# Optimization experiments

Measured on AMD Instinct MI355X. Metric: run time of the kernel, lower is better.

The kernel has to match this reference:

```python
import math
import jax, jax.numpy as jnp
import numpy as np

EMBED_DIM = 1024
NUM_HEADS = 16
HEAD_DIM = EMBED_DIM // NUM_HEADS


def _xavier(key, fan_in, fan_out):
    lim = math.sqrt(6.0 / (fan_in + fan_out))
    return jax.random.uniform(key, (fan_out, fan_in), jnp.float32, -lim, lim)


def setup_inputs() -> dict:
    key = jax.random.key(0)
    kx, kq, kk, kv, ko = jax.random.split(key, 5)
    B, L = 4, 2048
    x = jax.random.normal(kx, (B, L, EMBED_DIM), jnp.float32)
    return {
        "x": x,
        "wq": _xavier(kq, EMBED_DIM, EMBED_DIM), "bq": jnp.zeros((EMBED_DIM,), jnp.float32),
        "wk": _xavier(kk, EMBED_DIM, EMBED_DIM), "bk": jnp.zeros((EMBED_DIM,), jnp.float32),
        "wv": _xavier(kv, EMBED_DIM, EMBED_DIM), "bv": jnp.zeros((EMBED_DIM,), jnp.float32),
        "wo": _xavier(ko, EMBED_DIM, EMBED_DIM), "bo": jnp.zeros((EMBED_DIM,), jnp.float32),
    }


def reference(x, wq, bq, wk, bk, wv, bv, wo, bo):
    B, L, D = x.shape
    H, Dh = NUM_HEADS, HEAD_DIM

    def proj(w, b):
        # nn.Linear: x @ w.T + b, then split heads -> (B, H, L, Dh)
        return (jnp.einsum('bld,ed->ble', x, w) + b).reshape(B, L, H, Dh).transpose(0, 2, 1, 3)

    q, k, v = proj(wq, bq), proj(wk, bk), proj(wv, bv)
    # NOTE: original torch code scales by sqrt(key.size(dim=1)) == sqrt(num_heads)
    scale = 1.0 / math.sqrt(H)
    scores = jnp.einsum('bhqd,bhkd->bhqk', q, k) * scale  # (B, H, L, L)
    attn = jax.nn.softmax(scores, axis=-1)
    out = jnp.einsum('bhqk,bhkd->bhqd', attn, v)          # (B, H, L, Dh)
    out = out.transpose(0, 2, 1, 3).reshape(B, L, D)
    return jnp.einsum('bld,ed->ble', out, wo) + bo
```

## Files before the change

kernel.cpp:

```cpp
#include <hip/hip_runtime.h>
#include <hip/hip_bf16.h>

#define DEVI __device__ __forceinline__

using u16 = unsigned short;
typedef __attribute__((ext_vector_type(8))) short bf16x8;
typedef __attribute__((ext_vector_type(4))) short bf16x4;
typedef __attribute__((ext_vector_type(4))) float f32x4;

constexpr int Bb = 4, Ls = 2048, Dd = 1024, Hh = 16, DhC = 64;
constexpr int Mm = Bb * Ls;

DEVI u16 f2bf(float f) {
  union { float f; unsigned u; } x; x.f = f;
  unsigned r = x.u + 0x7FFFu + ((x.u >> 16) & 1u);
  return (u16)(r >> 16);
}
DEVI float bf2f(u16 b) {
  union { unsigned u; float f; } x; x.u = ((unsigned)b) << 16;
  return x.f;
}

DEVI unsigned cvt_pk_bf16(float a, float b) {
  unsigned d;
  asm("v_cvt_pk_bf16_f32 %0, %1, %2" : "=v"(d) : "v"(a), "v"(b));
  return d;
}

DEVI void gload_lds16(const u16* g, u16* l) {
  __builtin_amdgcn_global_load_lds(
      (const __attribute__((address_space(1))) unsigned int*)g,
      (__attribute__((address_space(3))) unsigned int*)l, 16, 0, 0);
}

DEVI bf16x8 ld_frag(const u16* p) { return *reinterpret_cast<const bf16x8*>(p); }

__global__ void cvt_all(const float* __restrict__ x,
                        const float* __restrict__ wq, const float* __restrict__ wk,
                        const float* __restrict__ wv, const float* __restrict__ wo,
                        u16* __restrict__ xb,
                        u16* __restrict__ wqb, u16* __restrict__ wkb,
                        u16* __restrict__ wvb, u16* __restrict__ wob) {
  const int tid = blockIdx.x * blockDim.x + threadIdx.x;
  constexpr int NT = 2048 * 256;
  constexpr int N4X = Mm * Dd / 4;
  constexpr int N4W = Dd * Dd / 4;
  for (int i = tid; i < N4X; i += NT) {
    float4 v = reinterpret_cast<const float4*>(x)[i];
    reinterpret_cast<ushort4*>(xb)[i] =
        make_ushort4(f2bf(v.x), f2bf(v.y), f2bf(v.z), f2bf(v.w));
  }
  for (int i = tid; i < 4 * N4W; i += NT) {
    int which = i / N4W, off = i - which * N4W;
    const float* s = which == 0 ? wq : which == 1 ? wk : which == 2 ? wv : wo;
    u16* d = which == 0 ? wqb : which == 1 ? wkb : which == 2 ? wvb : wob;
    float4 v = reinterpret_cast<const float4*>(s)[off];
    reinterpret_cast<ushort4*>(d)[off] =
        make_ushort4(f2bf(v.x), f2bf(v.y), f2bf(v.z), f2bf(v.w));
  }
}

__global__ __launch_bounds__(256) void gemm_qkv(
    const u16* __restrict__ A, const u16* __restrict__ W,
    const float* __restrict__ bq, const float* __restrict__ bk2,
    const float* __restrict__ bv,
    u16* __restrict__ qm, u16* __restrict__ km, u16* __restrict__ vt)
{
  constexpr int BK = 64, K = 1024;
  __shared__ u16 As[128 * BK];
  __shared__ u16 Bs[128 * BK];
  const int tid = threadIdx.x;
  const int wave = tid >> 6, lane = tid & 63;
  const int wr = wave >> 1, wc = wave & 1;
  const int lrow = lane & 15, lk = (lane >> 4) * 8;
  const int m0 = blockIdx.y * 128;
  const int n0g = blockIdx.x * 128;
  const int srow = lane >> 3, scol = (lane & 7) * 8;

  f32x4 acc[4][4] = {};

  for (int k0 = 0; k0 < K; k0 += BK) {
    __syncthreads();
#pragma unroll
    for (int i = 0; i < 4; ++i) {
      int g = wave * 4 + i;
      int row = g * 8 + srow;
      gload_lds16(A + (size_t)(m0 + row) * K + k0 + scol, As + g * 512);
      gload_lds16(W + (size_t)(n0g + row) * K + k0 + scol, Bs + g * 512);
    }
    __syncthreads();
#pragma unroll
    for (int kk = 0; kk < 2; ++kk) {
      bf16x8 af[4], bfr[4];
#pragma unroll
      for (int m = 0; m < 4; ++m) af[m]  = ld_frag(As + (wr*64 + m*16 + lrow)*BK + kk*32 + lk);
#pragma unroll
      for (int n = 0; n < 4; ++n) bfr[n] = ld_frag(Bs + (wc*64 + n*16 + lrow)*BK + kk*32 + lk);
      __builtin_amdgcn_s_setprio(1);
#pragma unroll
      for (int m = 0; m < 4; ++m)
#pragma unroll
        for (int n = 0; n < 4; ++n)
          acc[m][n] = __builtin_amdgcn_mfma_f32_16x16x32_bf16(af[m], bfr[n], acc[m][n], 0, 0, 0);
      __builtin_amdgcn_s_setprio(0);
    }
  }

  const int region = blockIdx.x >> 3;
  const int nc0 = (blockIdx.x & 7) * 128;
  const float* bias = region == 0 ? bq : region == 1 ? bk2 : bv;
  u16* dstRM = region == 0 ? qm : km;

#pragma unroll
  for (int m = 0; m < 4; ++m) {
#pragma unroll
    for (int n = 0; n < 4; ++n) {
      int row = m0 + wr*64 + m*16 + (lane >> 4) * 4;
      int col = nc0 + wc*64 + n*16 + lrow;
      float bv_ = bias[col];
      if (region == 2) {
        ushort4 o;
        o.x = f2bf(acc[m][n][0] + bv_); o.y = f2bf(acc[m][n][1] + bv_);
        o.z = f2bf(acc[m][n][2] + bv_); o.w = f2bf(acc[m][n][3] + bv_);
        *reinterpret_cast<ushort4*>(&vt[(size_t)col * Mm + row]) = o;
      } else {
#pragma unroll
        for (int j = 0; j < 4; ++j)
          dstRM[(size_t)(row + j) * Dd + col] = f2bf(acc[m][n][j] + bv_);
      }
    }
  }
}

__global__ __launch_bounds__(256) void gemm_out(
    const u16* __restrict__ A, const u16* __restrict__ Bt,
    const float* __restrict__ bias, float* __restrict__ C, int M, int N, int K)
{
  constexpr int BK = 64;
  __shared__ u16 As[128 * BK];
  __shared__ u16 Bs[128 * BK];
  const int tid = threadIdx.x;
  const int wave = tid >> 6, lane = tid & 63;
  const int wr = wave >> 1, wc = wave & 1;
  const int lrow = lane & 15, lk = (lane >> 4) * 8;
  const int m0 = blockIdx.y * 128, n0 = blockIdx.x * 128;
  const int srow = lane >> 3, scol = (lane & 7) * 8;

  f32x4 acc[4][4] = {};

  for (int k0 = 0; k0 < K; k0 += BK) {
    __syncthreads();
#pragma unroll
    for (int i = 0; i < 4; ++i) {
      int g = wave * 4 + i;
      int row = g * 8 + srow;
      gload_lds16(A  + (size_t)(m0 + row) * K + k0 + scol, As + g * 512);
      gload_lds16(Bt + (size_t)(n0 + row) * K + k0 + scol, Bs + g * 512);
    }
    __syncthreads();
#pragma unroll
    for (int kk = 0; kk < 2; ++kk) {
      bf16x8 af[4], bfr[4];
#pragma unroll
      for (int m = 0; m < 4; ++m) af[m]  = ld_frag(As + (wr*64 + m*16 + lrow)*BK + kk*32 + lk);
#pragma unroll
      for (int n = 0; n < 4; ++n) bfr[n] = ld_frag(Bs + (wc*64 + n*16 + lrow)*BK + kk*32 + lk);
      __builtin_amdgcn_s_setprio(1);
#pragma unroll
      for (int m = 0; m < 4; ++m)
#pragma unroll
        for (int n = 0; n < 4; ++n)
          acc[m][n] = __builtin_amdgcn_mfma_f32_16x16x32_bf16(af[m], bfr[n], acc[m][n], 0, 0, 0);
      __builtin_amdgcn_s_setprio(0);
    }
  }

#pragma unroll
  for (int m = 0; m < 4; ++m) {
#pragma unroll
    for (int n = 0; n < 4; ++n) {
      int row = m0 + wr*64 + m*16 + (lane >> 4) * 4;
      int col = n0 + wc*64 + n*16 + lrow;
      float bv = bias[col];
#pragma unroll
      for (int j = 0; j < 4; ++j)
        C[(size_t)(row + j) * N + col] = acc[m][n][j] + bv;
    }
  }
}

__global__ __launch_bounds__(512) void attn_fwd(
    const u16* __restrict__ Qm, const u16* __restrict__ Km,
    const u16* __restrict__ Vt, u16* __restrict__ Om)
{
  __shared__ u16 Ks[2][4096];
  __shared__ u16 Vs[2][4096];

  const int tid = threadIdx.x;
  const int wave = tid >> 6, lane = tid & 63;
  const int lrow = lane & 15, lk = (lane >> 4) * 8;
  const int swz = (lrow & 7) << 3;
  const int b = blockIdx.x >> 4, h = blockIdx.x & 15;
  const int rb = b * Ls;
  const int cb0 = h * DhC;
  const int q0 = blockIdx.y * 128;
  const int srow = lane >> 3;
  const int scol = ((lane & 7) ^ srow) * 8;

  const u16* kg = Km + (size_t)(rb + wave * 8 + srow) * Dd + cb0 + scol;
  const u16* vg = Vt + (size_t)(cb0 + wave * 8 + srow) * Mm + rb + scol;
  u16* ksflat = &Ks[0][0];
  u16* vsflat = &Vs[0][0];
  u16* ksl = ksflat + wave * 512;
  u16* vsl = vsflat + wave * 512;
  constexpr int LBUF = 4096;

#pragma unroll
  for (int g = 0; g < 2; ++g)
    gload_lds16(Qm + (size_t)(rb + q0 + wave * 16 + g * 8 + srow) * Dd + cb0 + scol,
                ksflat + (wave * 2 + g) * 512);
  gload_lds16(vg, vsl);
  __syncthreads();

  constexpr float SCL = 0.25f * 1.44269504088896f;
  bf16x8 aq0 = ld_frag(ksflat + (wave * 16 + lrow) * 64 + (lk ^ swz));
  bf16x8 aq1 = ld_frag(ksflat + (wave * 16 + lrow) * 64 + ((32 + lk) ^ swz));
#pragma unroll
  for (int e = 0; e < 8; e += 2) {
    unsigned d0 = cvt_pk_bf16(SCL * bf2f((u16)aq0[e]), SCL * bf2f((u16)aq0[e + 1]));
    unsigned d1 = cvt_pk_bf16(SCL * bf2f((u16)aq1[e]), SCL * bf2f((u16)aq1[e + 1]));
    aq0[e] = (short)(d0 & 0xffff); aq0[e + 1] = (short)(d0 >> 16);
    aq1[e] = (short)(d1 & 0xffff); aq1[e + 1] = (short)(d1 >> 16);
  }
  __syncthreads();
  gload_lds16(kg, ksl);
  __syncthreads();

  bf16x8 ones;
#pragma unroll
  for (int e = 0; e < 8; ++e) ones[e] = (short)0x3F80;

  f32x4 accO[4] = {};
  f32x4 acc_ps = {};

  int nb = 0;
  for (int kv0 = 0; kv0 < Ls; kv0 += 64) {
    if (kv0 + 64 < Ls) {
      int dst = (nb ^ 1) * LBUF;
      gload_lds16(kg + (size_t)(kv0 + 64) * Dd, ksl + dst);
      gload_lds16(vg + kv0 + 64, vsl + dst);
      asm volatile("s_waitcnt vmcnt(2)" ::: "memory");
    } else {
      asm volatile("s_waitcnt vmcnt(0)" ::: "memory");
    }
    __builtin_amdgcn_s_barrier();
    const u16* ks = ksflat + nb * LBUF;
    const u16* vs = vsflat + nb * LBUF;

    f32x4 s[4];
#pragma unroll
    for (int kb = 0; kb < 4; ++kb) {
      const u16* kr = ks + (kb * 16 + lrow) * 64;
      bf16x8 bk0 = ld_frag(kr + (lk ^ swz));
      bf16x8 bk1 = ld_frag(kr + ((32 + lk) ^ swz));
      f32x4 t = {};
      __builtin_amdgcn_s_setprio(1);
      t = __builtin_amdgcn_mfma_f32_16x16x32_bf16(bk0, aq0, t, 0, 0, 0);
      t = __builtin_amdgcn_mfma_f32_16x16x32_bf16(bk1, aq1, t, 0, 0, 0);
      __builtin_amdgcn_s_setprio(0);
      s[kb] = t;
    }

    unsigned u00 = cvt_pk_bf16(__builtin_amdgcn_exp2f(s[0][0]), __builtin_amdgcn_exp2f(s[0][1]));
    unsigned u01 = cvt_pk_bf16(__builtin_amdgcn_exp2f(s[0][2]), __builtin_amdgcn_exp2f(s[0][3]));
    unsigned u10 = cvt_pk_bf16(__builtin_amdgcn_exp2f(s[1][0]), __builtin_amdgcn_exp2f(s[1][1]));
    unsigned u11 = cvt_pk_bf16(__builtin_amdgcn_exp2f(s[1][2]), __builtin_amdgcn_exp2f(s[1][3]));
    unsigned u20 = cvt_pk_bf16(__builtin_amdgcn_exp2f(s[2][0]), __builtin_amdgcn_exp2f(s[2][1]));
    unsigned u21 = cvt_pk_bf16(__builtin_amdgcn_exp2f(s[2][2]), __builtin_amdgcn_exp2f(s[2][3]));
    unsigned u30 = cvt_pk_bf16(__builtin_amdgcn_exp2f(s[3][0]), __builtin_amdgcn_exp2f(s[3][1]));
    unsigned u31 = cvt_pk_bf16(__builtin_amdgcn_exp2f(s[3][2]), __builtin_amdgcn_exp2f(s[3][3]));

    asm("v_permlane32_swap_b32 %0, %1" : "+v"(u00), "+v"(u10));
    asm("v_permlane16_swap_b32 %0, %1" : "+v"(u00), "+v"(u10));
    asm("v_permlane32_swap_b32 %0, %1" : "+v"(u01), "+v"(u11));
    asm("v_permlane16_swap_b32 %0, %1" : "+v"(u01), "+v"(u11));
    asm("v_permlane32_swap_b32 %0, %1" : "+v"(u20), "+v"(u30));
    asm("v_permlane16_swap_b32 %0, %1" : "+v"(u20), "+v"(u30));
    asm("v_permlane32_swap_b32 %0, %1" : "+v"(u21), "+v"(u31));
    asm("v_permlane16_swap_b32 %0, %1" : "+v"(u21), "+v"(u31));

    union { unsigned u[4]; bf16x8 v; } apc0, apc1;
    apc0.u[0] = u00; apc0.u[1] = u01; apc0.u[2] = u10; apc0.u[3] = u11;
    apc1.u[0] = u20; apc1.u[1] = u21; apc1.u[2] = u30; apc1.u[3] = u31;

#pragma unroll
    for (int kk2 = 0; kk2 < 2; ++kk2) {
      bf16x8 ap = kk2 == 0 ? apc0.v : apc1.v;
      __builtin_amdgcn_s_setprio(1);
#pragma unroll
      for (int cb = 0; cb < 4; ++cb) {
        const u16* vr = vs + (cb * 16 + lrow) * 64;
        bf16x8 bv = ld_frag(vr + ((kk2 * 32 + lk) ^ swz));
        accO[cb] = __builtin_amdgcn_mfma_f32_16x16x32_bf16(bv, ap, accO[cb], 0, 0, 0);
      }
      acc_ps = __builtin_amdgcn_mfma_f32_16x16x32_bf16(ones, ap, acc_ps, 0, 0, 0);
      __builtin_amdgcn_s_setprio(0);
    }

    if (kv0 + 64 < Ls) __builtin_amdgcn_s_barrier();
    nb ^= 1;
  }

  float rinv = 1.0f / acc_ps[0];
  const size_t orow = (size_t)(rb + q0 + wave * 16 + lrow) * Dd + cb0;
#pragma unroll
  for (int cb = 0; cb < 4; ++cb) {
    uint2 o;
    o.x = cvt_pk_bf16(accO[cb][0] * rinv, accO[cb][1] * rinv);
    o.y = cvt_pk_bf16(accO[cb][2] * rinv, accO[cb][3] * rinv);
    *reinterpret_cast<uint2*>(&Om[orow + cb * 16 + (lk >> 1)]) = o;
  }
}

extern "C" void kernel_launch(void* const* d_in, const int* in_sizes, int n_in,
                              void* d_out, int out_size, void* d_ws, size_t ws_size,
                              hipStream_t stream) {
  (void)in_sizes; (void)n_in; (void)out_size; (void)ws_size;
  const float* x  = (const float*)d_in[0];
  const float* wq = (const float*)d_in[1];
  const float* bq = (const float*)d_in[2];
  const float* wk = (const float*)d_in[3];
  const float* bk = (const float*)d_in[4];
  const float* wv = (const float*)d_in[5];
  const float* bv = (const float*)d_in[6];
  const float* wo = (const float*)d_in[7];
  const float* bo = (const float*)d_in[8];
  float* out = (float*)d_out;

  u16* ws  = (u16*)d_ws;
  u16* xb  = ws;
  u16* wqb = xb  + (size_t)Mm * Dd;
  u16* wkb = wqb + (size_t)Dd * Dd;
  u16* wvb = wkb + (size_t)Dd * Dd;
  u16* wob = wvb + (size_t)Dd * Dd;
  u16* qm  = wob + (size_t)Dd * Dd;
  u16* km  = qm  + (size_t)Mm * Dd;
  u16* vt  = km  + (size_t)Mm * Dd;
  u16* om  = xb;

  cvt_all<<<2048, 256, 0, stream>>>(x, wq, wk, wv, wo, xb, wqb, wkb, wvb, wob);

  dim3 qkvgrid(3 * Dd / 128, Mm / 128);
  gemm_qkv<<<qkvgrid, 256, 0, stream>>>(xb, wqb, bq, bk, bv, qm, km, vt);

  dim3 agrid(Bb * Hh, Ls / 128);
  attn_fwd<<<agrid, 512, 0, stream>>>(qm, km, vt, om);

  dim3 ogrid(Dd / 128, Mm / 128);
  gemm_out<<<ogrid, 256, 0, stream>>>(om, wob, bo, out, Mm, Dd, Dd);
}
```

Baseline: 207.0 us.

## Rewrite QKV GEMM as 256x256 tile with double-buffered swizzled LDS pipeline

Replaces the 128x128 QKV projection GEMM with a 256x256 tile kernel using 512 threads, a double-buffered LDS ring with XOR-swizzled layout, and staged prefetch of the next K-slice interleaved with four MFMA sub-phases. The aim is to overlap global loads with compute, raise data reuse per block, and avoid LDS bank conflicts. The grid shrinks to 12x32 blocks, which may hurt occupancy and load balance across CUs. The larger tile also increases LDS use (128KB) and register pressure.

```diff
diff --git a/kernel.cpp b/kernel.cpp
--- a/kernel.cpp
+++ b/kernel.cpp
@@ -60,73 +60,157 @@
   }
 }
 
-__global__ __launch_bounds__(256) void gemm_qkv(
+__global__ __launch_bounds__(512) void gemm_qkv256(
     const u16* __restrict__ A, const u16* __restrict__ W,
     const float* __restrict__ bq, const float* __restrict__ bk2,
     const float* __restrict__ bv,
     u16* __restrict__ qm, u16* __restrict__ km, u16* __restrict__ vt)
 {
-  constexpr int BK = 64, K = 1024;
-  __shared__ u16 As[128 * BK];
-  __shared__ u16 Bs[128 * BK];
+  constexpr int K = 1024, BK = 64, NSTEP = K / BK;
+  __shared__ u16 lds[2][2][256 * 64];
+
   const int tid = threadIdx.x;
   const int wave = tid >> 6, lane = tid & 63;
-  const int wr = wave >> 1, wc = wave & 1;
-  const int lrow = lane & 15, lk = (lane >> 4) * 8;
-  const int m0 = blockIdx.y * 128;
-  const int n0g = blockIdx.x * 128;
-  const int srow = lane >> 3, scol = (lane & 7) * 8;
-
-  f32x4 acc[4][4] = {};
-
-  for (int k0 = 0; k0 < K; k0 += BK) {
-    __syncthreads();
-#pragma unroll
-    for (int i = 0; i < 4; ++i) {
-      int g = wave * 4 + i;
-      int row = g * 8 + srow;
-      gload_lds16(A + (size_t)(m0 + row) * K + k0 + scol, As + g * 512);
-      gload_lds16(W + (size_t)(n0g + row) * K + k0 + scol, Bs + g * 512);
-    }
-    __syncthreads();
-#pragma unroll
-    for (int kk = 0; kk < 2; ++kk) {
-      bf16x8 af[4], bfr[4];
-#pragma unroll
-      for (int m = 0; m < 4; ++m) af[m]  = ld_frag(As + (wr*64 + m*16 + lrow)*BK + kk*32 + lk);
-#pragma unroll
-      for (int n = 0; n < 4; ++n) bfr[n] = ld_frag(Bs + (wc*64 + n*16 + lrow)*BK + kk*32 + lk);
-      __builtin_amdgcn_s_setprio(1);
-#pragma unroll
-      for (int m = 0; m < 4; ++m)
-#pragma unroll
-        for (int n = 0; n < 4; ++n)
-          acc[m][n] = __builtin_amdgcn_mfma_f32_16x16x32_bf16(af[m], bfr[n], acc[m][n], 0, 0, 0);
-      __builtin_amdgcn_s_setprio(0);
-    }
-  }
-
-  const int region = blockIdx.x >> 3;
-  const int nc0 = (blockIdx.x & 7) * 128;
+  const int wr = wave >> 2, wc = wave & 3;
+  const int lrow = lane & 15, hi = lane >> 4, lk = hi * 8;
+  const int swz = (lrow & 7) << 3;
+  const int m0 = blockIdx.y * 256;
+  const int n0g = blockIdx.x * 256;
+
+  const int c_row[4] = { (0*512 + tid) >> 3, (1*512 + tid) >> 3,
+                         (2*512 + tid) >> 3, (3*512 + tid) >> 3 };
+  int c_kc[4];
+#pragma unroll
+  for (int p = 0; p < 4; ++p)
+    c_kc[p] = (((p * 512 + tid) & 7) ^ (c_row[p] & 7)) * 8;
+
+  f32x4 acc[8][4] = {};
+
+#pragma unroll
+  for (int p = 0; p < 4; ++p) {
+    int c = p * 512 + tid;
+    gload_lds16(A + (size_t)(m0 + c_row[p]) * K + c_kc[p], &lds[0][0][0] + c * 8);
+    gload_lds16(W + (size_t)(n0g + c_row[p]) * K + c_kc[p], &lds[0][1][0] + c * 8);
+  }
+  __syncthreads();
+
+  for (int t = 0; t < NSTEP; ++t) {
+    const u16* Ab = &lds[t & 1][0][0];
+    const u16* Bb = &lds[t & 1][1][0];
+    u16* An = &lds[(t + 1) & 1][0][0];
+    u16* Bn = &lds[(t + 1) & 1][1][0];
+    const int k1 = (t + 1) * BK;
+    const bool more = (t + 1 < NSTEP);
+
+    bf16x8 a[4][2], b0[2][2], b1[2][2];
+
+#define STAGE_Q(p)                                                             \
+    if (more) {                                                                \
+      int c = (p) * 512 + tid;                                                 \
+      gload_lds16(A + (size_t)(m0 + c_row[p]) * K + k1 + c_kc[p], An + c * 8); \
+      gload_lds16(W + (size_t)(n0g + c_row[p]) * K + k1 + c_kc[p], Bn + c * 8);\
+    }
+
+#pragma unroll
+    for (int f = 0; f < 4; ++f) {
+      int row = wr * 128 + f * 16 + lrow;
+      a[f][0] = ld_frag(Ab + row * 64 + (lk ^ swz));
+      a[f][1] = ld_frag(Ab + row * 64 + ((32 + lk) ^ swz));
+    }
+#pragma unroll
+    for (int f = 0; f < 2; ++f) {
+      int row = wc * 64 + f * 16 + lrow;
+      b0[f][0] = ld_frag(Bb + row * 64 + (lk ^ swz));
+      b0[f][1] = ld_frag(Bb + row * 64 + ((32 + lk) ^ swz));
+    }
+    STAGE_Q(0);
+    __builtin_amdgcn_s_barrier();
+    __builtin_amdgcn_s_setprio(1);
+#pragma unroll
+    for (int fm = 0; fm < 4; ++fm)
+#pragma unroll
+      for (int fn = 0; fn < 2; ++fn)
+#pragma unroll
+        for (int kk = 0; kk < 2; ++kk)
+          acc[fm][fn] = __builtin_amdgcn_mfma_f32_16x16x32_bf16(a[fm][kk], b0[fn][kk], acc[fm][fn], 0, 0, 0);
+    __builtin_amdgcn_s_setprio(0);
+    __builtin_amdgcn_s_barrier();
+
+#pragma unroll
+    for (int f = 0; f < 2; ++f) {
+      int row = wc * 64 + (2 + f) * 16 + lrow;
+      b1[f][0] = ld_frag(Bb + row * 64 + (lk ^ swz));
+      b1[f][1] = ld_frag(Bb + row * 64 + ((32 + lk) ^ swz));
+    }
+    STAGE_Q(1);
+    __builtin_amdgcn_s_barrier();
+    __builtin_amdgcn_s_setprio(1);
+#pragma unroll
+    for (int fm = 0; fm < 4; ++fm)
+#pragma unroll
+      for (int fn = 0; fn < 2; ++fn)
+#pragma unroll
+        for (int kk = 0; kk < 2; ++kk)
+          acc[fm][2 + fn] = __builtin_amdgcn_mfma_f32_16x16x32_bf16(a[fm][kk], b1[fn][kk], acc[fm][2 + fn], 0, 0, 0);
+    __builtin_amdgcn_s_setprio(0);
+    __builtin_amdgcn_s_barrier();
+
+#pragma unroll
+    for (int f = 0; f < 4; ++f) {
+      int row = wr * 128 + (4 + f) * 16 + lrow;
+      a[f][0] = ld_frag(Ab + row * 64 + (lk ^ swz));
+      a[f][1] = ld_frag(Ab + row * 64 + ((32 + lk) ^ swz));
+    }
+    STAGE_Q(2);
+    __builtin_amdgcn_s_barrier();
+    __builtin_amdgcn_s_setprio(1);
+#pragma unroll
+    for (int fm = 0; fm < 4; ++fm)
+#pragma unroll
+      for (int fn = 0; fn < 2; ++fn)
+#pragma unroll
+        for (int kk = 0; kk < 2; ++kk)
+          acc[4 + fm][2 + fn] = __builtin_amdgcn_mfma_f32_16x16x32_bf16(a[fm][kk], b1[fn][kk], acc[4 + fm][2 + fn], 0, 0, 0);
+    __builtin_amdgcn_s_setprio(0);
+    __builtin_amdgcn_s_barrier();
+
+    STAGE_Q(3);
+    __builtin_amdgcn_s_barrier();
+    __builtin_amdgcn_s_setprio(1);
+#pragma unroll
+    for (int fm = 0; fm < 4; ++fm)
+#pragma unroll
+      for (int fn = 0; fn < 2; ++fn)
+#pragma unroll
+        for (int kk = 0; kk < 2; ++kk)
+          acc[4 + fm][fn] = __builtin_amdgcn_mfma_f32_16x16x32_bf16(a[fm][kk], b0[fn][kk], acc[4 + fm][fn], 0, 0, 0);
+    __builtin_amdgcn_s_setprio(0);
+    if (more) asm volatile("s_waitcnt vmcnt(0)" ::: "memory");
+    __builtin_amdgcn_s_barrier();
+#undef STAGE_Q
+  }
+
+  const int region = blockIdx.x >> 2;
+  const int nc0 = (blockIdx.x & 3) * 256;
   const float* bias = region == 0 ? bq : region == 1 ? bk2 : bv;
   u16* dstRM = region == 0 ? qm : km;
 
 #pragma unroll
-  for (int m = 0; m < 4; ++m) {
-#pragma unroll
-    for (int n = 0; n < 4; ++n) {
-      int row = m0 + wr*64 + m*16 + (lane >> 4) * 4;
-      int col = nc0 + wc*64 + n*16 + lrow;
+  for (int fm = 0; fm < 8; ++fm) {
+#pragma unroll
+    for (int fn = 0; fn < 4; ++fn) {
+      int row = m0 + wr * 128 + fm * 16 + hi * 4;
+      int col = nc0 + wc * 64 + fn * 16 + lrow;
       float bv_ = bias[col];
       if (region == 2) {
         ushort4 o;
-        o.x = f2bf(acc[m][n][0] + bv_); o.y = f2bf(acc[m][n][1] + bv_);
-        o.z = f2bf(acc[m][n][2] + bv_); o.w = f2bf(acc[m][n][3] + bv_);
+        o.x = f2bf(acc[fm][fn][0] + bv_); o.y = f2bf(acc[fm][fn][1] + bv_);
+        o.z = f2bf(acc[fm][fn][2] + bv_); o.w = f2bf(acc[fm][fn][3] + bv_);
         *reinterpret_cast<ushort4*>(&vt[(size_t)col * Mm + row]) = o;
       } else {
 #pragma unroll
         for (int j = 0; j < 4; ++j)
-          dstRM[(size_t)(row + j) * Dd + col] = f2bf(acc[m][n][j] + bv_);
+          dstRM[(size_t)(row + j) * Dd + col] = f2bf(acc[fm][fn][j] + bv_);
       }
     }
   }
@@ -350,8 +434,8 @@
 
   cvt_all<<<2048, 256, 0, stream>>>(x, wq, wk, wv, wo, xb, wqb, wkb, wvb, wob);
 
-  dim3 qkvgrid(3 * Dd / 128, Mm / 128);
-  gemm_qkv<<<qkvgrid, 256, 0, stream>>>(xb, wqb, bq, bk, bv, qm, km, vt);
+  dim3 qkvgrid(3 * Dd / 256, Mm / 256);
+  gemm_qkv256<<<qkvgrid, 512, 0, stream>>>(xb, wqb, bq, bk, bv, qm, km, vt);
 
   dim3 agrid(Bb * Hh, Ls / 128);
   attn_fwd<<<agrid, 512, 0, stream>>>(qm, km, vt, om);
```

After: 197.2 us. -4.7%, faster.
